# Optimization experiments

Measured on AMD Instinct MI355X. Metric: run time of the kernel, lower is better.

The kernel has to match this reference:

```python
import jax, jax.numpy as jnp
import numpy as np

N = 100000   # nodes
E = 1600000  # edges
IN = 64      # in_channels
H = 128      # hidden_features
G = 1024     # graphs in batch
NUM_REST = 3 # num_layers (extra GraphConv layers)


def setup_inputs() -> dict:
    key = jax.random.key(0)
    ks = jax.random.split(key, 12)
    x = jax.random.normal(ks[0], (N, IN), jnp.float32)
    edge_index = jax.random.randint(ks[1], (2, E), 0, N)
    edge_attr = jax.random.uniform(ks[2], (E,), jnp.float32)
    batch = jnp.sort(jax.random.randint(ks[3], (N,), 0, G))

    def glorot(k, shape, fan_in):
        return jax.random.normal(k, shape, jnp.float32) / np.float32(np.sqrt(fan_in))

    # GraphConv layer 0: in -> hidden (lin_root: no bias, lin_rel: bias)
    W_root0 = glorot(ks[4], (H, IN), IN)
    W_rel0 = glorot(ks[5], (H, IN), IN)
    b0 = jnp.zeros((H,), jnp.float32)
    # GraphConv layers 1..3: hidden -> hidden (stacked)
    W_root_r = glorot(ks[6], (NUM_REST, H, H), H)
    W_rel_r = glorot(ks[7], (NUM_REST, H, H), H)
    b_r = jnp.zeros((NUM_REST, H), jnp.float32)
    # MLPReadout: [H -> H//2 -> 1]
    Wr1 = glorot(ks[8], (H // 2, H), H)
    br1 = jnp.zeros((H // 2,), jnp.float32)
    Wr2 = glorot(ks[9], (1, H // 2), H // 2)
    br2 = jnp.zeros((1,), jnp.float32)
    return dict(x=x, edge_index=edge_index, edge_attr=edge_attr, batch=batch,
                W_root0=W_root0, W_rel0=W_rel0, b0=b0,
                W_root_r=W_root_r, W_rel_r=W_rel_r, b_r=b_r,
                Wr1=Wr1, br1=br1, Wr2=Wr2, br2=br2)


def graph_conv(x, src, dst, ew, W_root, W_rel, b):
    # PyG GraphConv (aggr='add'):
    #   out_i = W_rel @ sum_{j->i} e_ji * x_j + b + W_root @ x_i
    msg = ew[:, None] * x[src]                                   # [E, d]
    agg = jax.ops.segment_sum(msg, dst, num_segments=x.shape[0])  # [N, d]
    return agg @ W_rel.T + b + x @ W_root.T


def reference(x, edge_index, edge_attr, batch,
              W_root0, W_rel0, b0, W_root_r, W_rel_r, b_r,
              Wr1, br1, Wr2, br2):
    src, dst = edge_index[0], edge_index[1]
    y = graph_conv(x, src, dst, edge_attr, W_root0, W_rel0, b0)
    for l in range(W_root_r.shape[0]):
        y = graph_conv(y, src, dst, edge_attr, W_root_r[l], W_rel_r[l], b_r[l])
    # MLPReadout: Linear -> ReLU -> Linear
    y = jax.nn.relu(y @ Wr1.T + br1)
    y = y @ Wr2.T + br2                                           # [N, 1]
    # scatter-mean over graph assignment
    num = jax.ops.segment_sum(y, batch, num_segments=G)           # [G, 1]
    cnt = jax.ops.segment_sum(jnp.ones((y.shape[0], 1), y.dtype), batch,
                              num_segments=G)
    return num / jnp.maximum(cnt, 1.0)                            # [G, 1]
```

## Files before the change

kernel.cpp:

```cpp
#include <hip/hip_runtime.h>
#include <hip/hip_fp16.h>
#include <cstdint>
#include <cstddef>

#define NNODES 100000
#define NEDGES 1600000
#define NGRAPH 1024

#define BK 256
#define NBUCKET 391
#define CHUNK 4096
#define NCHUNK 391
#define NBE (NBUCKET * NCHUNK)

typedef __attribute__((ext_vector_type(8))) short short8;
typedef __attribute__((ext_vector_type(8))) unsigned short ushort8;
typedef __attribute__((ext_vector_type(4))) float f32x4;

__device__ inline float b2f(unsigned short u) {
  return __uint_as_float(((unsigned int)u) << 16);
}
__device__ inline unsigned short f2b(float f) {
  unsigned int x = __float_as_uint(f);
  x += 0x7fffu + ((x >> 16) & 1u);
  return (unsigned short)(x >> 16);
}
__device__ inline unsigned int pack_edge(int src, float w) {
  unsigned short hb = __half_as_ushort(__float2half_rn(w));
  return ((unsigned int)src << 15) | ((unsigned int)hb >> 1);
}
__device__ inline void unpack_edge(unsigned int p, int& src, float& w) {
  src = (int)(p >> 15);
  w = __half2float(__ushort_as_half((unsigned short)((p & 0x7fffu) << 1)));
}

__global__ __launch_bounds__(256) void prepack_kernel(
    const float* __restrict__ Wrel0, const float* __restrict__ Wroot0,
    const float* __restrict__ WrelR, const float* __restrict__ WrootR,
    const float* __restrict__ Wr1, unsigned short* __restrict__ dst)
{
  int g = blockIdx.x * 256 + threadIdx.x;
  if (g >= 15360) return;
  const float* src; int H, K, r; unsigned short* out;
  if (g < 1024)       { src = Wrel0;  H = 128; K = 64;  r = g;        out = dst + r * 8; }
  else if (g < 2048)  { src = Wroot0; H = 128; K = 64;  r = g - 1024; out = dst + 8192 + r * 8; }
  else if (g < 8192)  { int m = g - 2048; int l = m / 2048; r = m % 2048;
                        src = WrelR + l * 16384;  H = 128; K = 128;
                        out = dst + 16384 + l * 16384 + r * 8; }
  else if (g < 14336) { int m = g - 8192; int l = m / 2048; r = m % 2048;
                        src = WrootR + l * 16384; H = 128; K = 128;
                        out = dst + 65536 + l * 16384 + r * 8; }
  else                { src = Wr1;    H = 64;  K = 128; r = g - 14336; out = dst + 114688 + r * 8; }
  int n = r % H, k8 = r / H;
  const float* s = src + (size_t)n * K + k8 * 8;
#pragma unroll
  for (int j = 0; j < 8; j++) out[j] = f2b(s[j]);
}

__global__ __launch_bounds__(256) void cvt_x_kernel(
    const float* __restrict__ x, unsigned short* __restrict__ xb)
{
  int i = blockIdx.x * 256 + threadIdx.x;
  if (i * 4 >= NNODES * 64) return;
  float4 v = *(const float4*)(x + i * 4);
  ushort4 o;
  o.x = f2b(v.x); o.y = f2b(v.y); o.z = f2b(v.z); o.w = f2b(v.w);
  *(ushort4*)(xb + i * 4) = o;
}

__global__ __launch_bounds__(256) void bucket_count_kernel(
    const int* __restrict__ ei, int* __restrict__ cnt)
{
  __shared__ int hist[NBUCKET];
  for (int i = threadIdx.x; i < NBUCKET; i += 256) hist[i] = 0;
  __syncthreads();
  int base = blockIdx.x * CHUNK;
  for (int t = threadIdx.x; t < CHUNK; t += 256) {
    int e = base + t;
    if (e < NEDGES) atomicAdd(&hist[ei[NEDGES + e] >> 8], 1);
  }
  __syncthreads();
  for (int i = threadIdx.x; i < NBUCKET; i += 256)
    cnt[i * NCHUNK + blockIdx.x] = hist[i];
}

__global__ __launch_bounds__(512) void row_scan_kernel(
    int* __restrict__ cnt, int* __restrict__ rowsum)
{
  __shared__ int s[512];
  int b = blockIdx.x, t = threadIdx.x;
  int v = (t < NCHUNK) ? cnt[b * NCHUNK + t] : 0;
  s[t] = v;
  __syncthreads();
#pragma unroll
  for (int off = 1; off < 512; off <<= 1) {
    int u = (t >= off) ? s[t - off] : 0;
    __syncthreads();
    s[t] += u;
    __syncthreads();
  }
  if (t < NCHUNK) cnt[b * NCHUNK + t] = s[t] - v;
  if (t == 511) rowsum[b] = s[511];
}

__global__ __launch_bounds__(512) void rowbase_scan_kernel(
    const int* __restrict__ rowsum, int* __restrict__ rowbase)
{
  __shared__ int s[512];
  int t = threadIdx.x;
  int v = (t < NBUCKET) ? rowsum[t] : 0;
  s[t] = v;
  __syncthreads();
#pragma unroll
  for (int off = 1; off < 512; off <<= 1) {
    int u = (t >= off) ? s[t - off] : 0;
    __syncthreads();
    s[t] += u;
    __syncthreads();
  }
  if (t < NBUCKET) rowbase[t] = s[t] - v;
  if (t == 511) rowbase[NBUCKET] = s[511];
}

__global__ __launch_bounds__(256) void bucket_scatter_kernel(
    const int* __restrict__ ei, const float* __restrict__ ew,
    const int* __restrict__ cnt, const int* __restrict__ rowbase,
    uint2* __restrict__ rec)
{
  __shared__ int pos[NBUCKET];
  for (int i = threadIdx.x; i < NBUCKET; i += 256)
    pos[i] = rowbase[i] + cnt[i * NCHUNK + blockIdx.x];
  __syncthreads();
  int base = blockIdx.x * CHUNK;
  for (int t = threadIdx.x; t < CHUNK; t += 256) {
    int e = base + t;
    if (e < NEDGES) {
      int d = ei[NEDGES + e];
      int p = atomicAdd(&pos[d >> 8], 1);
      rec[p] = make_uint2((unsigned int)d, pack_edge(ei[e], ew[e]));
    }
  }
}

__global__ __launch_bounds__(256) void bucket_fill_kernel(
    const int* __restrict__ rowbase, const uint2* __restrict__ rec,
    unsigned int* __restrict__ epack, int* __restrict__ row_ptr)
{
  __shared__ int off[BK];
  __shared__ int s[256];
  int b = blockIdx.x, t = threadIdx.x;
  int start = rowbase[b];
  int end = rowbase[b + 1];
  int nbase = b * BK;
  off[t] = 0;
  __syncthreads();
  for (int i = start + t; i < end; i += 256)
    atomicAdd(&off[rec[i].x - nbase], 1);
  __syncthreads();
  int v = off[t];
  s[t] = v;
  __syncthreads();
#pragma unroll
  for (int o = 1; o < 256; o <<= 1) {
    int u = (t >= o) ? s[t - o] : 0;
    __syncthreads();
    s[t] += u;
    __syncthreads();
  }
  int ex = s[t] - v;
  int g = nbase + t;
  if (g <= NNODES) row_ptr[g] = start + ex;
  __syncthreads();
  off[t] = ex;
  __syncthreads();
  for (int i = start + t; i < end; i += 256) {
    uint2 r = rec[i];
    int lp = atomicAdd(&off[r.x - nbase], 1);
    epack[start + lp] = r.y;
  }
}

__global__ __launch_bounds__(256) void gptr_kernel(
    const int* __restrict__ batch, int* __restrict__ gptr)
{
  int i = blockIdx.x * 256 + threadIdx.x;
  if (i >= NNODES) return;
  int b = batch[i];
  int bn = (i + 1 < NNODES) ? batch[i + 1] : NGRAPH;
  for (int g = b + 1; g <= bn; g++) gptr[g] = i + 1;
  if (i == 0) for (int g = 0; g <= b; g++) gptr[g] = 0;
}

__global__ __launch_bounds__(256) void agg128_kernel(
    const int* __restrict__ row_ptr, const unsigned int* __restrict__ epack,
    const unsigned short* __restrict__ x, unsigned short* __restrict__ agg)
{
  __shared__ float part[4][128];
  const int wave = threadIdx.x >> 6, lane = threadIdx.x & 63;
  const int node = blockIdx.x * 2 + (wave >> 1);
  const int half = wave & 1;
  const int q = lane >> 4, sl = lane & 15;
  int s = row_ptr[node], e = row_ptr[node + 1];
  float acc[8];
#pragma unroll
  for (int j = 0; j < 8; j++) acc[j] = 0.f;

  for (int i = s + half * 16 + q; i < e; i += 32) {
    unsigned int p0 = epack[i];
    unsigned int p1 = (i + 4  < e) ? epack[i + 4]  : 0u;
    unsigned int p2 = (i + 8  < e) ? epack[i + 8]  : 0u;
    unsigned int p3 = (i + 12 < e) ? epack[i + 12] : 0u;
    int s0, s1, s2, s3; float w0, w1, w2, w3;
    unpack_edge(p0, s0, w0);
    unpack_edge(p1, s1, w1);
    unpack_edge(p2, s2, w2);
    unpack_edge(p3, s3, w3);
    ushort8 r0 = *(const ushort8*)(x + (size_t)s0 * 128 + sl * 8);
    ushort8 r1 = *(const ushort8*)(x + (size_t)s1 * 128 + sl * 8);
    ushort8 r2 = *(const ushort8*)(x + (size_t)s2 * 128 + sl * 8);
    ushort8 r3 = *(const ushort8*)(x + (size_t)s3 * 128 + sl * 8);
#pragma unroll
    for (int j = 0; j < 8; j++)
      acc[j] += w0 * b2f(r0[j]) + w1 * b2f(r1[j]) +
                w2 * b2f(r2[j]) + w3 * b2f(r3[j]);
  }
#pragma unroll
  for (int j = 0; j < 8; j++) {
    acc[j] += __shfl_xor(acc[j], 16, 64);
    acc[j] += __shfl_xor(acc[j], 32, 64);
  }
  if (q == 0) {
#pragma unroll
    for (int j = 0; j < 8; j++) part[wave][sl * 8 + j] = acc[j];
  }
  __syncthreads();
  if (half == 0 && q == 0) {
    ushort8 o;
#pragma unroll
    for (int j = 0; j < 8; j++)
      o[j] = f2b(part[wave][sl * 8 + j] + part[wave + 1][sl * 8 + j]);
    *(ushort8*)(agg + (size_t)node * 128 + sl * 8) = o;
  }
}

__global__ __launch_bounds__(256) void agg64_kernel(
    const int* __restrict__ row_ptr, const unsigned int* __restrict__ epack,
    const unsigned short* __restrict__ x, unsigned short* __restrict__ agg)
{
  __shared__ float part[4][64];
  const int wave = threadIdx.x >> 6, lane = threadIdx.x & 63;
  const int node = blockIdx.x * 2 + (wave >> 1);
  const int half = wave & 1;
  const int q = lane >> 3, sl = lane & 7;
  int s = row_ptr[node], e = row_ptr[node + 1];
  float acc[8];
#pragma unroll
  for (int j = 0; j < 8; j++) acc[j] = 0.f;

  for (int i = s + half * 16 + q; i < e; i += 32) {
    unsigned int p0 = epack[i];
    unsigned int p1 = (i + 8 < e) ? epack[i + 8] : 0u;
    int s0, s1; float w0, w1;
    unpack_edge(p0, s0, w0);
    unpack_edge(p1, s1, w1);
    ushort8 r0 = *(const ushort8*)(x + (size_t)s0 * 64 + sl * 8);
    ushort8 r1 = *(const ushort8*)(x + (size_t)s1 * 64 + sl * 8);
#pragma unroll
    for (int j = 0; j < 8; j++)
      acc[j] += w0 * b2f(r0[j]) + w1 * b2f(r1[j]);
  }
#pragma unroll
  for (int j = 0; j < 8; j++) {
    acc[j] += __shfl_xor(acc[j], 8, 64);
    acc[j] += __shfl_xor(acc[j], 16, 64);
    acc[j] += __shfl_xor(acc[j], 32, 64);
  }
  if (q == 0) {
#pragma unroll
    for (int j = 0; j < 8; j++) part[wave][sl * 8 + j] = acc[j];
  }
  __syncthreads();
  if (half == 0 && q == 0) {
    ushort8 o;
#pragma unroll
    for (int j = 0; j < 8; j++)
      o[j] = f2b(part[wave][sl * 8 + j] + part[wave + 1][sl * 8 + j]);
    *(ushort8*)(agg + (size_t)node * 64 + sl * 8) = o;
  }
}

template <int KDIM, int HOUT, int MT, bool DUAL, bool RELU>
__global__ __launch_bounds__(256) void mfma_gemm(
    const unsigned short* __restrict__ A1, const unsigned short* __restrict__ W1,
    const unsigned short* __restrict__ A2, const unsigned short* __restrict__ W2,
    const float* __restrict__ bias, unsigned short* __restrict__ out)
{
  constexpr int NT2 = HOUT / 16;
  constexpr int KC = KDIM / 32;
  const int wave = threadIdx.x >> 6, lane = threadIdx.x & 63;
  const int quad = lane >> 4, l16 = lane & 15;
  const int n0 = (blockIdx.x * 4 + wave) * (MT * 16);

  f32x4 acc[MT][NT2];
#pragma unroll
  for (int m = 0; m < MT; m++)
#pragma unroll
    for (int t = 0; t < NT2; t++) acc[m][t] = (f32x4){0.f, 0.f, 0.f, 0.f};

  int nodes[MT];
#pragma unroll
  for (int m = 0; m < MT; m++) {
    int nd = n0 + m * 16 + l16;
    nodes[m] = nd < NNODES ? nd : NNODES - 1;
  }

#pragma unroll
  for (int c = 0; c < KC; c++) {
    short8 bfr[NT2];
#pragma unroll
    for (int t = 0; t < NT2; t++)
      bfr[t] = *(const short8*)(W1 + ((size_t)(c * 4 + quad) * HOUT + t * 16 + l16) * 8);
#pragma unroll
    for (int m = 0; m < MT; m++) {
      short8 af = *(const short8*)(A1 + (size_t)nodes[m] * KDIM + c * 32 + quad * 8);
#pragma unroll
      for (int t = 0; t < NT2; t++)
        acc[m][t] = __builtin_amdgcn_mfma_f32_16x16x32_bf16(af, bfr[t], acc[m][t], 0, 0, 0);
    }
    if (DUAL) {
#pragma unroll
      for (int t = 0; t < NT2; t++)
        bfr[t] = *(const short8*)(W2 + ((size_t)(c * 4 + quad) * HOUT + t * 16 + l16) * 8);
#pragma unroll
      for (int m = 0; m < MT; m++) {
        short8 af = *(const short8*)(A2 + (size_t)nodes[m] * KDIM + c * 32 + quad * 8);
#pragma unroll
        for (int t = 0; t < NT2; t++)
          acc[m][t] = __builtin_amdgcn_mfma_f32_16x16x32_bf16(af, bfr[t], acc[m][t], 0, 0, 0);
      }
    }
  }

#pragma unroll
  for (int m = 0; m < MT; m++) {
    int rowbase = n0 + m * 16 + quad * 4;
#pragma unroll
    for (int t = 0; t < NT2; t++) {
      float b = bias[t * 16 + l16];
#pragma unroll
      for (int r = 0; r < 4; r++) {
        int nd = rowbase + r;
        if (nd < NNODES) {
          float v = acc[m][t][r] + b;
          if (RELU) v = fmaxf(v, 0.f);
          out[(size_t)nd * HOUT + t * 16 + l16] = f2b(v);
        }
      }
    }
  }
}

__global__ __launch_bounds__(256) void readout_fused_kernel(
    const unsigned short* __restrict__ A1, const unsigned short* __restrict__ W1,
    const float* __restrict__ br1, const float* __restrict__ Wr2,
    const int* __restrict__ batch, float* __restrict__ gnum)
{
  constexpr int NT2 = 4, KC = 4, MT = 4;
  const int wave = threadIdx.x >> 6, lane = threadIdx.x & 63;
  const int quad = lane >> 4, l16 = lane & 15;
  const int n0 = (blockIdx.x * 4 + wave) * (MT * 16);

  f32x4 acc[MT][NT2];
#pragma unroll
  for (int m = 0; m < MT; m++)
#pragma unroll
    for (int t = 0; t < NT2; t++) acc[m][t] = (f32x4){0.f, 0.f, 0.f, 0.f};

  int nodes[MT];
#pragma unroll
  for (int m = 0; m < MT; m++) {
    int nd = n0 + m * 16 + l16;
    nodes[m] = nd < NNODES ? nd : NNODES - 1;
  }

#pragma unroll
  for (int c = 0; c < KC; c++) {
    short8 bfr[NT2];
#pragma unroll
    for (int t = 0; t < NT2; t++)
      bfr[t] = *(const short8*)(W1 + ((size_t)(c * 4 + quad) * 64 + t * 16 + l16) * 8);
#pragma unroll
    for (int m = 0; m < MT; m++) {
      short8 af = *(const short8*)(A1 + (size_t)nodes[m] * 128 + c * 32 + quad * 8);
#pragma unroll
      for (int t = 0; t < NT2; t++)
        acc[m][t] = __builtin_amdgcn_mfma_f32_16x16x32_bf16(af, bfr[t], acc[m][t], 0, 0, 0);
    }
  }

  float bv[NT2], wv[NT2];
#pragma unroll
  for (int t = 0; t < NT2; t++) {
    bv[t] = br1[t * 16 + l16];
    wv[t] = Wr2[t * 16 + l16];
  }
#pragma unroll
  for (int m = 0; m < MT; m++) {
    int rowbase = n0 + m * 16 + quad * 4;
#pragma unroll
    for (int r = 0; r < 4; r++) {
      float p = 0.f;
#pragma unroll
      for (int t = 0; t < NT2; t++)
        p += fmaxf(acc[m][t][r] + bv[t], 0.f) * wv[t];
      p += __shfl_xor(p, 1, 64);
      p += __shfl_xor(p, 2, 64);
      p += __shfl_xor(p, 4, 64);
      p += __shfl_xor(p, 8, 64);
      int nd = rowbase + r;
      if (l16 == 0 && nd < NNODES)
        atomicAdd(&gnum[batch[nd]], p);
    }
  }
}

__global__ __launch_bounds__(256) void finalize_kernel(
    const float* __restrict__ gnum, const int* __restrict__ gptr,
    const float* __restrict__ br2, float* __restrict__ out)
{
  int g = blockIdx.x * 256 + threadIdx.x;
  if (g >= NGRAPH) return;
  float cnt = (float)(gptr[g + 1] - gptr[g]);
  out[g] = (gnum[g] + cnt * br2[0]) / fmaxf(cnt, 1.f);
}

extern "C" void kernel_launch(void* const* d_in, const int* in_sizes, int n_in,
                              void* d_out, int out_size, void* d_ws, size_t ws_size,
                              hipStream_t stream)
{
  const float* x      = (const float*)d_in[0];
  const int*   ei     = (const int*)d_in[1];
  const float* ew     = (const float*)d_in[2];
  const int*   batch  = (const int*)d_in[3];
  const float* Wroot0 = (const float*)d_in[4];
  const float* Wrel0  = (const float*)d_in[5];
  const float* b0     = (const float*)d_in[6];
  const float* WrootR = (const float*)d_in[7];
  const float* WrelR  = (const float*)d_in[8];
  const float* bR     = (const float*)d_in[9];
  const float* Wr1    = (const float*)d_in[10];
  const float* br1    = (const float*)d_in[11];
  const float* Wr2    = (const float*)d_in[12];
  const float* br2    = (const float*)d_in[13];

  char* ws = (char*)d_ws;
  unsigned short* wp   = (unsigned short*)ws;
  unsigned short* xb   = wp + 131072;
  unsigned short* agg0 = xb + (size_t)NNODES * 64;
  unsigned short* bufA = agg0 + (size_t)NNODES * 64;
  unsigned short* bufB = bufA + (size_t)NNODES * 128;
  unsigned short* hbuf = bufB + (size_t)NNODES * 128;
  int*  cnt      = (int*)(hbuf + (size_t)NNODES * 64);
  int*  rowsum   = cnt + ((NBE + 63) & ~63);
  int*  rowbase  = rowsum + NBUCKET + 1;
  int*  row_ptr  = rowbase + NBUCKET + 1;
  int*  gptr     = row_ptr + NNODES + 2;
  unsigned int* epack = (unsigned int*)(gptr + NGRAPH + 2);
  uint2* rec = (uint2*)bufA;
  float* gnum = (float*)hbuf;

  prepack_kernel<<<60, 256, 0, stream>>>(Wrel0, Wroot0, WrelR, WrootR, Wr1, wp);
  cvt_x_kernel<<<(NNODES * 64 / 4 + 255) / 256, 256, 0, stream>>>(x, xb);
  hipMemsetAsync(gnum, 0, NGRAPH * sizeof(float), stream);

  const unsigned short* pWrel0  = wp;
  const unsigned short* pWroot0 = wp + 8192;
  const unsigned short* pWrelR  = wp + 16384;
  const unsigned short* pWrootR = wp + 65536;
  const unsigned short* pWr1    = wp + 114688;

  bucket_count_kernel<<<NCHUNK, 256, 0, stream>>>(ei, cnt);
  row_scan_kernel<<<NBUCKET, 512, 0, stream>>>(cnt, rowsum);
  rowbase_scan_kernel<<<1, 512, 0, stream>>>(rowsum, rowbase);
  bucket_scatter_kernel<<<NCHUNK, 256, 0, stream>>>(ei, ew, cnt, rowbase, rec);
  bucket_fill_kernel<<<NBUCKET, 256, 0, stream>>>(rowbase, rec, epack, row_ptr);
  gptr_kernel<<<(NNODES + 255) / 256, 256, 0, stream>>>(batch, gptr);

  agg64_kernel<<<NNODES / 2, 256, 0, stream>>>(row_ptr, epack, xb, agg0);
  mfma_gemm<64, 128, 2, true, false><<<(NNODES + 127) / 128, 256, 0, stream>>>(
      agg0, pWrel0, xb, pWroot0, b0, bufB);

  unsigned short* bufs[2] = { bufB, bufA };
  for (int l = 0; l < 3; l++) {
    unsigned short* in  = bufs[l & 1];
    unsigned short* agg = bufs[(l & 1) ^ 1];
    agg128_kernel<<<NNODES / 2, 256, 0, stream>>>(row_ptr, epack, in, agg);
    mfma_gemm<128, 128, 2, true, false><<<(NNODES + 127) / 128, 256, 0, stream>>>(
        agg, pWrelR + l * 16384, in, pWrootR + l * 16384, bR + l * 128, agg);
  }

  readout_fused_kernel<<<(NNODES + 255) / 256, 256, 0, stream>>>(
      bufA, pWr1, br1, Wr2, batch, gnum);
  finalize_kernel<<<(NGRAPH + 255) / 256, 256, 0, stream>>>(gnum, gptr, br2, (float*)d_out);
}
```

Baseline: 589.0 us.

## Fuse setup kernels into one launch and use one wave per node in aggregation

Folds the x conversion, weight prepack, graph-pointer build, bucket count and the gnum memset into a single block-partitioned setup kernel, cutting several launches and a memset. The aggregation kernels now give each node a single wavefront instead of splitting its edges across two waves joined through shared memory and a barrier. This removes LDS traffic and __syncthreads, but each wave walks twice as many edges in sequence, which can lengthen per-node latency.

After: 524.0 us. 1.12x faster.

```diff
diff --git a/kernel.cpp b/kernel.cpp
--- a/kernel.cpp
+++ b/kernel.cpp
@@ -13,6 +13,12 @@
 #define NCHUNK 391
 #define NBE (NBUCKET * NCHUNK)
 
+#define SB_CVT 6250
+#define SB_PRE (SB_CVT + 60)
+#define SB_GPTR (SB_PRE + 391)
+#define SB_CNT (SB_GPTR + NCHUNK)
+#define SB_TOTAL (SB_CNT + 1)
+
 typedef __attribute__((ext_vector_type(8))) short short8;
 typedef __attribute__((ext_vector_type(8))) unsigned short ushort8;
 typedef __attribute__((ext_vector_type(4))) float f32x4;
@@ -34,54 +40,63 @@
   w = __half2float(__ushort_as_half((unsigned short)((p & 0x7fffu) << 1)));
 }
 
-__global__ __launch_bounds__(256) void prepack_kernel(
+__global__ __launch_bounds__(256) void setup_kernel(
+    const float* __restrict__ x, unsigned short* __restrict__ xb,
     const float* __restrict__ Wrel0, const float* __restrict__ Wroot0,
     const float* __restrict__ WrelR, const float* __restrict__ WrootR,
-    const float* __restrict__ Wr1, unsigned short* __restrict__ dst)
-{
-  int g = blockIdx.x * 256 + threadIdx.x;
-  if (g >= 15360) return;
-  const float* src; int H, K, r; unsigned short* out;
-  if (g < 1024)       { src = Wrel0;  H = 128; K = 64;  r = g;        out = dst + r * 8; }
-  else if (g < 2048)  { src = Wroot0; H = 128; K = 64;  r = g - 1024; out = dst + 8192 + r * 8; }
-  else if (g < 8192)  { int m = g - 2048; int l = m / 2048; r = m % 2048;
-                        src = WrelR + l * 16384;  H = 128; K = 128;
-                        out = dst + 16384 + l * 16384 + r * 8; }
-  else if (g < 14336) { int m = g - 8192; int l = m / 2048; r = m % 2048;
-                        src = WrootR + l * 16384; H = 128; K = 128;
-                        out = dst + 65536 + l * 16384 + r * 8; }
-  else                { src = Wr1;    H = 64;  K = 128; r = g - 14336; out = dst + 114688 + r * 8; }
-  int n = r % H, k8 = r / H;
-  const float* s = src + (size_t)n * K + k8 * 8;
-#pragma unroll
-  for (int j = 0; j < 8; j++) out[j] = f2b(s[j]);
-}
-
-__global__ __launch_bounds__(256) void cvt_x_kernel(
-    const float* __restrict__ x, unsigned short* __restrict__ xb)
-{
-  int i = blockIdx.x * 256 + threadIdx.x;
-  if (i * 4 >= NNODES * 64) return;
-  float4 v = *(const float4*)(x + i * 4);
-  ushort4 o;
-  o.x = f2b(v.x); o.y = f2b(v.y); o.z = f2b(v.z); o.w = f2b(v.w);
-  *(ushort4*)(xb + i * 4) = o;
-}
-
-__global__ __launch_bounds__(256) void bucket_count_kernel(
-    const int* __restrict__ ei, int* __restrict__ cnt)
+    const float* __restrict__ Wr1, unsigned short* __restrict__ wp,
+    const int* __restrict__ batch, int* __restrict__ gptr,
+    const int* __restrict__ ei, int* __restrict__ cnt,
+    float* __restrict__ gnum)
 {
   __shared__ int hist[NBUCKET];
-  for (int i = threadIdx.x; i < NBUCKET; i += 256) hist[i] = 0;
-  __syncthreads();
-  int base = blockIdx.x * CHUNK;
-  for (int t = threadIdx.x; t < CHUNK; t += 256) {
-    int e = base + t;
-    if (e < NEDGES) atomicAdd(&hist[ei[NEDGES + e] >> 8], 1);
-  }
-  __syncthreads();
-  for (int i = threadIdx.x; i < NBUCKET; i += 256)
-    cnt[i * NCHUNK + blockIdx.x] = hist[i];
+  int blk = blockIdx.x;
+  if (blk < SB_CVT) {
+    int i = blk * 256 + threadIdx.x;
+    float4 v = *(const float4*)(x + (size_t)i * 4);
+    ushort4 o;
+    o.x = f2b(v.x); o.y = f2b(v.y); o.z = f2b(v.z); o.w = f2b(v.w);
+    *(ushort4*)(xb + (size_t)i * 4) = o;
+  } else if (blk < SB_PRE) {
+    int g = (blk - SB_CVT) * 256 + threadIdx.x;
+    if (g >= 15360) return;
+    const float* src; int H, K, r; unsigned short* out;
+    if (g < 1024)       { src = Wrel0;  H = 128; K = 64;  r = g;        out = wp + r * 8; }
+    else if (g < 2048)  { src = Wroot0; H = 128; K = 64;  r = g - 1024; out = wp + 8192 + r * 8; }
+    else if (g < 8192)  { int m = g - 2048; int l = m / 2048; r = m % 2048;
+                          src = WrelR + l * 16384;  H = 128; K = 128;
+                          out = wp + 16384 + l * 16384 + r * 8; }
+    else if (g < 14336) { int m = g - 8192; int l = m / 2048; r = m % 2048;
+                          src = WrootR + l * 16384; H = 128; K = 128;
+                          out = wp + 65536 + l * 16384 + r * 8; }
+    else                { src = Wr1;    H = 64;  K = 128; r = g - 14336; out = wp + 114688 + r * 8; }
+    int n = r % H, k8 = r / H;
+    const float* s = src + (size_t)n * K + k8 * 8;
+#pragma unroll
+    for (int j = 0; j < 8; j++) out[j] = f2b(s[j]);
+  } else if (blk < SB_GPTR) {
+    int i = (blk - SB_PRE) * 256 + threadIdx.x;
+    if (i >= NNODES) return;
+    int b = batch[i];
+    int bn = (i + 1 < NNODES) ? batch[i + 1] : NGRAPH;
+    for (int g = b + 1; g <= bn; g++) gptr[g] = i + 1;
+    if (i == 0) for (int g = 0; g <= b; g++) gptr[g] = 0;
+  } else if (blk < SB_CNT) {
+    int chunk = blk - SB_GPTR;
+    for (int i = threadIdx.x; i < NBUCKET; i += 256) hist[i] = 0;
+    __syncthreads();
+    int base = chunk * CHUNK;
+    for (int t = threadIdx.x; t < CHUNK; t += 256) {
+      int e = base + t;
+      if (e < NEDGES) atomicAdd(&hist[ei[NEDGES + e] >> 8], 1);
+    }
+    __syncthreads();
+    for (int i = threadIdx.x; i < NBUCKET; i += 256)
+      cnt[i * NCHUNK + chunk] = hist[i];
+  } else {
+#pragma unroll
+    for (int j = 0; j < 4; j++) gnum[threadIdx.x + j * 256] = 0.f;
+  }
 }
 
 __global__ __launch_bounds__(512) void row_scan_kernel(
@@ -180,32 +195,20 @@
   }
 }
 
-__global__ __launch_bounds__(256) void gptr_kernel(
-    const int* __restrict__ batch, int* __restrict__ gptr)
-{
-  int i = blockIdx.x * 256 + threadIdx.x;
-  if (i >= NNODES) return;
-  int b = batch[i];
-  int bn = (i + 1 < NNODES) ? batch[i + 1] : NGRAPH;
-  for (int g = b + 1; g <= bn; g++) gptr[g] = i + 1;
-  if (i == 0) for (int g = 0; g <= b; g++) gptr[g] = 0;
-}
-
 __global__ __launch_bounds__(256) void agg128_kernel(
     const int* __restrict__ row_ptr, const unsigned int* __restrict__ epack,
     const unsigned short* __restrict__ x, unsigned short* __restrict__ agg)
 {
-  __shared__ float part[4][128];
-  const int wave = threadIdx.x >> 6, lane = threadIdx.x & 63;
-  const int node = blockIdx.x * 2 + (wave >> 1);
-  const int half = wave & 1;
-  const int q = lane >> 4, sl = lane & 15;
+  int node = blockIdx.x * 4 + (threadIdx.x >> 6);
+  int lane = threadIdx.x & 63;
+  if (node >= NNODES) return;
+  int q = lane >> 4, sl = lane & 15;
   int s = row_ptr[node], e = row_ptr[node + 1];
   float acc[8];
 #pragma unroll
   for (int j = 0; j < 8; j++) acc[j] = 0.f;
 
-  for (int i = s + half * 16 + q; i < e; i += 32) {
+  for (int i = s + q; i < e; i += 16) {
     unsigned int p0 = epack[i];
     unsigned int p1 = (i + 4  < e) ? epack[i + 4]  : 0u;
     unsigned int p2 = (i + 8  < e) ? epack[i + 8]  : 0u;
@@ -230,15 +233,9 @@
     acc[j] += __shfl_xor(acc[j], 32, 64);
   }
   if (q == 0) {
-#pragma unroll
-    for (int j = 0; j < 8; j++) part[wave][sl * 8 + j] = acc[j];
-  }
-  __syncthreads();
-  if (half == 0 && q == 0) {
     ushort8 o;
 #pragma unroll
-    for (int j = 0; j < 8; j++)
-      o[j] = f2b(part[wave][sl * 8 + j] + part[wave + 1][sl * 8 + j]);
+    for (int j = 0; j < 8; j++) o[j] = f2b(acc[j]);
     *(ushort8*)(agg + (size_t)node * 128 + sl * 8) = o;
   }
 }
@@ -247,17 +244,16 @@
     const int* __restrict__ row_ptr, const unsigned int* __restrict__ epack,
     const unsigned short* __restrict__ x, unsigned short* __restrict__ agg)
 {
-  __shared__ float part[4][64];
-  const int wave = threadIdx.x >> 6, lane = threadIdx.x & 63;
-  const int node = blockIdx.x * 2 + (wave >> 1);
-  const int half = wave & 1;
-  const int q = lane >> 3, sl = lane & 7;
+  int node = blockIdx.x * 4 + (threadIdx.x >> 6);
+  int lane = threadIdx.x & 63;
+  if (node >= NNODES) return;
+  int q = lane >> 3, sl = lane & 7;
   int s = row_ptr[node], e = row_ptr[node + 1];
   float acc[8];
 #pragma unroll
   for (int j = 0; j < 8; j++) acc[j] = 0.f;
 
-  for (int i = s + half * 16 + q; i < e; i += 32) {
+  for (int i = s + q; i < e; i += 16) {
     unsigned int p0 = epack[i];
     unsigned int p1 = (i + 8 < e) ? epack[i + 8] : 0u;
     int s0, s1; float w0, w1;
@@ -276,15 +272,9 @@
     acc[j] += __shfl_xor(acc[j], 32, 64);
   }
   if (q == 0) {
-#pragma unroll
-    for (int j = 0; j < 8; j++) part[wave][sl * 8 + j] = acc[j];
-  }
-  __syncthreads();
-  if (half == 0 && q == 0) {
     ushort8 o;
 #pragma unroll
-    for (int j = 0; j < 8; j++)
-      o[j] = f2b(part[wave][sl * 8 + j] + part[wave + 1][sl * 8 + j]);
+    for (int j = 0; j < 8; j++) o[j] = f2b(acc[j]);
     *(ushort8*)(agg + (size_t)node * 64 + sl * 8) = o;
   }
 }
@@ -469,24 +459,21 @@
   uint2* rec = (uint2*)bufA;
   float* gnum = (float*)hbuf;
 
-  prepack_kernel<<<60, 256, 0, stream>>>(Wrel0, Wroot0, WrelR, WrootR, Wr1, wp);
-  cvt_x_kernel<<<(NNODES * 64 / 4 + 255) / 256, 256, 0, stream>>>(x, xb);
-  hipMemsetAsync(gnum, 0, NGRAPH * sizeof(float), stream);
-
   const unsigned short* pWrel0  = wp;
   const unsigned short* pWroot0 = wp + 8192;
   const unsigned short* pWrelR  = wp + 16384;
   const unsigned short* pWrootR = wp + 65536;
   const unsigned short* pWr1    = wp + 114688;
 
-  bucket_count_kernel<<<NCHUNK, 256, 0, stream>>>(ei, cnt);
+  setup_kernel<<<SB_TOTAL, 256, 0, stream>>>(
+      x, xb, Wrel0, Wroot0, WrelR, WrootR, Wr1, wp, batch, gptr, ei, cnt, gnum);
+
   row_scan_kernel<<<NBUCKET, 512, 0, stream>>>(cnt, rowsum);
   rowbase_scan_kernel<<<1, 512, 0, stream>>>(rowsum, rowbase);
   bucket_scatter_kernel<<<NCHUNK, 256, 0, stream>>>(ei, ew, cnt, rowbase, rec);
   bucket_fill_kernel<<<NBUCKET, 256, 0, stream>>>(rowbase, rec, epack, row_ptr);
-  gptr_kernel<<<(NNODES + 255) / 256, 256, 0, stream>>>(batch, gptr);
-
-  agg64_kernel<<<NNODES / 2, 256, 0, stream>>>(row_ptr, epack, xb, agg0);
+
+  agg64_kernel<<<(NNODES + 3) / 4, 256, 0, stream>>>(row_ptr, epack, xb, agg0);
   mfma_gemm<64, 128, 2, true, false><<<(NNODES + 127) / 128, 256, 0, stream>>>(
       agg0, pWrel0, xb, pWroot0, b0, bufB);
 
@@ -494,7 +481,7 @@
   for (int l = 0; l < 3; l++) {
     unsigned short* in  = bufs[l & 1];
     unsigned short* agg = bufs[(l & 1) ^ 1];
-    agg128_kernel<<<NNODES / 2, 256, 0, stream>>>(row_ptr, epack, in, agg);
+    agg128_kernel<<<(NNODES + 3) / 4, 256, 0, stream>>>(row_ptr, epack, in, agg);
     mfma_gemm<128, 128, 2, true, false><<<(NNODES + 127) / 128, 256, 0, stream>>>(
         agg, pWrelR + l * 16384, in, pWrootR + l * 16384, bR + l * 128, agg);
   }
```
